# Optimization experiments

Measured on AMD Instinct MI355X. Metric: run time of the kernel, lower is better.

The kernel has to match this reference:

```python
import jax, jax.numpy as jnp
import numpy as np

B, T, D = 4, 2048, 1024
DK, DV = 1024, 1024
BETA1, BETA2 = 1.0, 1.0
EPS = 1e-12  # torch F.normalize eps


def setup_inputs() -> dict:
    key = jax.random.key(0)
    kx, kq, kk, kv, ko = jax.random.split(key, 5)
    def w(k, shape):
        return jax.random.normal(k, shape, dtype=jnp.float32) * (shape[0] ** -0.5)
    return {
        "x": jax.random.normal(kx, (B, T, D), dtype=jnp.float32),
        # Weights stored [in, out]; torch Linear is x @ W.T with W [out, in] -- equivalent math.
        "Wq": w(kq, (D, DK)),
        "Wk": w(kk, (D, DK)),
        "Wv": w(kv, (D, DV)),
        "Wo": w(ko, (DV, D)),
    }


def reference(x, Wq, Wk, Wv, Wo):
    scale = DK ** -0.5
    q = (x @ Wq) * scale                      # [B,T,DK]
    k = x @ Wk
    k = k / jnp.maximum(jnp.linalg.norm(k, axis=-1, keepdims=True), EPS)
    v = x @ Wv                                # [B,T,DV]
    # time-major for scan
    qT = jnp.swapaxes(q, 0, 1)
    kT = jnp.swapaxes(k, 0, 1)
    vT = jnp.swapaxes(v, 0, 1)
    S0 = jnp.zeros((B, DV, DK), dtype=x.dtype)

    def step(S, qkv_t):
        q_t, k_t, v_t = qkv_t                 # each [B, d]
        # S @ (I - b1 k k^T) = S - b1 (S k) k^T   (same math, rank-1 form)
        Sk = jnp.einsum('bvk,bk->bv', S, k_t)
        S = S - BETA1 * Sk[:, :, None] * k_t[:, None, :] \
              + BETA2 * v_t[:, :, None] * k_t[:, None, :]
        o_t = jnp.einsum('bvk,bk->bv', S, q_t)
        return S, o_t

    _, oT = jax.lax.scan(step, S0, (qT, kT, vT))  # oT: [T,B,DV]
    out = jnp.swapaxes(oT, 0, 1) @ Wo             # [B,T,D]
    return out
```

## Files before the change

kernel.cpp:

```cpp
#include <hip/hip_runtime.h>

typedef unsigned short u16;
typedef __attribute__((ext_vector_type(8))) short short8;
typedef __attribute__((ext_vector_type(4))) float floatx4;

#define B_ 4
#define T_ 2048
#define CH 64

__device__ __forceinline__ u16 f2bf(float f) {
  unsigned int x = __float_as_uint(f);
  return (u16)((x + 0x7FFFu + ((x >> 16) & 1u)) >> 16);
}
__device__ __forceinline__ float bf2f(u16 u) {
  union { unsigned int i; float f; } v; v.i = ((unsigned int)u) << 16; return v.f;
}

__device__ __forceinline__ void barrier_lgkm() {
  asm volatile("s_waitcnt lgkmcnt(0)\n\ts_barrier" ::: "memory");
}

#define GL(dst, addr, IMM) \
  asm volatile("global_load_dwordx4 %0, %1, off offset:" #IMM : "=v"(dst) : "v"(addr))
#define GLU(dst, addr, IMM) \
  asm volatile("global_load_ushort %0, %1, off offset:" #IMM : "=v"(dst) : "v"(addr))
#define GS(addr, val, IMM) \
  asm volatile("global_store_short %0, %1, off offset:" #IMM :: "v"(addr), "v"(val))

#define GLA(slot, base, I0, I1, I2, I3) do { \
  GL(af[slot][0], base, I0); GL(af[slot][1], base, I1); \
  GL(af[slot][2], base, I2); GL(af[slot][3], base, I3); } while (0)

#define GLKT(nt0) do { \
  const u16* kp0_ = ktb + (size_t)(nt0) * ktstep; \
  GL(ktf[nt0][0], kp0_, 0); GL(ktf[nt0][1], kp0_, 64); \
  const u16* kp1_ = ktb + (size_t)(nt0 + 1) * ktstep; \
  GL(ktf[nt0 + 1][0], kp1_, 0); GL(ktf[nt0 + 1][1], kp1_, 64); } while (0)

#define GLX4 do { \
  GL(wpf0, wrow, 0); GL(wpf1, wrow, 64); \
  GLU(vv0, vvb, 0); GLU(vv1, vvb, 2048); \
  GLU(vv2, vvb2, 0); GLU(vv3, vvb2, 2048); } while (0)

#define NOOP ((void)0)

#define AITER(K, NW, PREFETCH, XCODE) do { \
  asm volatile("s_waitcnt vmcnt(" #NW ")"); \
  __builtin_amdgcn_sched_barrier(0x387); \
  PREFETCH; \
  XCODE; \
  short8 b0_ = *reinterpret_cast<const short8*>(&Sb[l16][(K * 4 + 0) * 32 + quad * 8]); \
  short8 b1_ = *reinterpret_cast<const short8*>(&Sb[l16][(K * 4 + 1) * 32 + quad * 8]); \
  short8 b2_ = *reinterpret_cast<const short8*>(&Sb[l16][(K * 4 + 2) * 32 + quad * 8]); \
  short8 b3_ = *reinterpret_cast<const short8*>(&Sb[l16][(K * 4 + 3) * 32 + quad * 8]); \
  ac0 = __builtin_amdgcn_mfma_f32_16x16x32_bf16(af[K][0], b0_, ac0, 0, 0, 0); \
  ac1 = __builtin_amdgcn_mfma_f32_16x16x32_bf16(af[K][1], b1_, ac1, 0, 0, 0); \
  ac2 = __builtin_amdgcn_mfma_f32_16x16x32_bf16(af[K][2], b2_, ac2, 0, 0, 0); \
  ac3 = __builtin_amdgcn_mfma_f32_16x16x32_bf16(af[K][3], b3_, ac3, 0, 0, 0); \
} while (0)

__global__ __launch_bounds__(256) void xconv_kernel(const float* __restrict__ x,
                                                    u16* __restrict__ Xbf) {
  size_t idx = ((size_t)blockIdx.x * 256 + threadIdx.x) * 4;
  float4 v = *reinterpret_cast<const float4*>(&x[idx]);
  ushort4 o;
  o.x = f2bf(v.x); o.y = f2bf(v.y); o.z = f2bf(v.z); o.w = f2bf(v.w);
  *reinterpret_cast<ushort4*>(&Xbf[idx]) = o;
}

__global__ __launch_bounds__(256) void wtrans_kernel(
    const float* __restrict__ W0, const float* __restrict__ W1,
    const float* __restrict__ W2, const float* __restrict__ W3,
    u16* __restrict__ T0, u16* __restrict__ T1,
    u16* __restrict__ T2, u16* __restrict__ T3)
{
  const int z = blockIdx.z;
  const float* W = (z == 0) ? W0 : (z == 1) ? W1 : (z == 2) ? W2 : W3;
  u16* T = (z == 0) ? T0 : (z == 1) ? T1 : (z == 2) ? T2 : T3;
  const int k0 = blockIdx.x * 64, n0 = blockIdx.y * 64;
  const int tid = threadIdx.x;
  __shared__ float Tile[64][65];
#pragma unroll
  for (int i = 0; i < 4; ++i) {
    int lin = tid + i * 256;
    int r = lin >> 4, c4 = (lin & 15) * 4;
    *reinterpret_cast<float4*>(&Tile[r][c4]) =
        *reinterpret_cast<const float4*>(&W[(size_t)(k0 + r) * 1024 + n0 + c4]);
  }
  __syncthreads();
#pragma unroll
  for (int i = 0; i < 4; ++i) {
    int lin = tid + i * 256;
    int r = lin >> 4, c4 = (lin & 15) * 4;
    ushort4 o;
    o.x = f2bf(Tile[c4 + 0][r]); o.y = f2bf(Tile[c4 + 1][r]);
    o.z = f2bf(Tile[c4 + 2][r]); o.w = f2bf(Tile[c4 + 3][r]);
    *reinterpret_cast<ushort4*>(&T[(size_t)(n0 + r) * 1024 + k0 + c4]) = o;
  }
}

__global__ __launch_bounds__(256) void mgemm_qkv(
    const u16* __restrict__ Xbf,
    const u16* __restrict__ WqT, const u16* __restrict__ WkT, const u16* __restrict__ WvT,
    u16* __restrict__ Qbf, u16* __restrict__ Kbf, u16* __restrict__ Vbf,
    int tg, int lsh)
{
  const int z = blockIdx.z;
  const u16* BT = (z == 0) ? WqT : ((z == 1) ? WkT : WvT);
  u16* O = (z == 0) ? Qbf : ((z == 1) ? Kbf : Vbf);
  const float scale = (z == 0) ? 0.03125f : 1.0f;
  const int r0 = blockIdx.x * 128, c0 = blockIdx.y * 128;
// ... 100 lines not shown
        int col = c0 + wc + ni * 16 + l16;
        out[(size_t)grow * 1024 + col] = acc[mi][ni][reg];
      }
    }
}

__global__ __launch_bounds__(256) void knorm_kernel(u16* __restrict__ Kbf) {
  const int row = blockIdx.x;
  const int tid = threadIdx.x;
  ushort4 v4 = *reinterpret_cast<const ushort4*>(&Kbf[(size_t)row * 1024 + tid * 4]);
  float a = bf2f(v4.x), b = bf2f(v4.y), c = bf2f(v4.z), d = bf2f(v4.w);
  float ss = a * a + b * b + c * c + d * d;
#pragma unroll
  for (int off = 32; off > 0; off >>= 1) ss += __shfl_down(ss, off);
  __shared__ float wsum[4];
  if ((tid & 63) == 0) wsum[tid >> 6] = ss;
  __syncthreads();
  float tot = wsum[0] + wsum[1] + wsum[2] + wsum[3];
  float inv = 1.0f / fmaxf(sqrtf(tot), 1e-12f);
  ushort4 o;
  o.x = f2bf(a * inv); o.y = f2bf(b * inv); o.z = f2bf(c * inv); o.w = f2bf(d * inv);
  *reinterpret_cast<ushort4*>(&Kbf[(size_t)row * 1024 + tid * 4]) = o;
}

__global__ __launch_bounds__(256) void ktrans_kernel(const u16* __restrict__ Kbf,
                                                     u16* __restrict__ KT,
                                                     int tgs) {
  const int t0 = blockIdx.x * 64;
  const int d0 = blockIdx.y * 64;
  const int b = blockIdx.z;
  const int tid = threadIdx.x;
  __shared__ u16 Tile[64][68];
#pragma unroll
  for (int i = 0; i < 4; ++i) {
    int lin = tid + i * 256;
    int r = lin >> 4, c4 = (lin & 15) * 4;
    *reinterpret_cast<ushort4*>(&Tile[r][c4]) =
        *reinterpret_cast<const ushort4*>(&Kbf[(size_t)(b * tgs + t0 + r) * 1024 + d0 + c4]);
  }
  __syncthreads();
#pragma unroll
  for (int i = 0; i < 4; ++i) {
    int lin = tid + i * 256;
    int r = lin >> 4, c4 = (lin & 15) * 4;
    ushort4 o;
    o.x = Tile[c4 + 0][r]; o.y = Tile[c4 + 1][r];
    o.z = Tile[c4 + 2][r]; o.w = Tile[c4 + 3][r];
    *reinterpret_cast<ushort4*>(&KT[((size_t)b * 1024 + d0 + r) * tgs + t0 + c4]) = o;
  }
}

__global__ __launch_bounds__(256) void attn_winv_kernel(
    const u16* __restrict__ Qbf, const u16* __restrict__ Kbf,
    u16* __restrict__ Pb, u16* __restrict__ Wb, int tgs)
{
  const int cc = blockIdx.x;
  const int b = blockIdx.y;
  const int base = b * tgs + cc * CH;
  const int tid = threadIdx.x;
  const int lane = tid & 63;
  const int wave = tid >> 6;
  const int quad = lane >> 4, l16 = lane & 15;
  const int m0 = wave * 16;

  __shared__ float Asm[64][64];
  __shared__ float Wsm[64][65];

  floatx4 accA[4] = {};
  floatx4 accP[4] = {};
  const u16* arowK = &Kbf[(size_t)(base + m0 + l16) * 1024];
  const u16* arowQ = &Qbf[(size_t)(base + m0 + l16) * 1024];
#pragma unroll 4
  for (int kk = 0; kk < 32; ++kk) {
    short8 aK = *reinterpret_cast<const short8*>(&arowK[kk * 32 + quad * 8]);
    short8 aQ = *reinterpret_cast<const short8*>(&arowQ[kk * 32 + quad * 8]);
#pragma unroll
    for (int nt = 0; nt < 4; ++nt) {
      short8 bK = *reinterpret_cast<const short8*>(
          &Kbf[(size_t)(base + nt * 16 + l16) * 1024 + kk * 32 + quad * 8]);
      accA[nt] = __builtin_amdgcn_mfma_f32_16x16x32_bf16(aK, bK, accA[nt], 0, 0, 0);
      accP[nt] = __builtin_amdgcn_mfma_f32_16x16x32_bf16(aQ, bK, accP[nt], 0, 0, 0);
    }
  }
  const size_t pw0 = ((size_t)(cc * B_ + b) * CH) * 64;
#pragma unroll
  for (int nt = 0; nt < 4; ++nt) {
#pragma unroll
    for (int reg = 0; reg < 4; ++reg) {
      int t = m0 + quad * 4 + reg;
      int i = nt * 16 + l16;
      Asm[t][i] = (i < t) ? accA[nt][reg] : 0.0f;
      Pb[pw0 + (size_t)t * 64 + i] = f2bf((i <= t) ? accP[nt][reg] : 0.0f);
    }
  }
  __syncthreads();

  if (tid < 64) {
    const int j = tid;
    for (int t = 0; t < 64; ++t) {
      float s = (t == j) ? 1.0f : 0.0f;
      for (int i = 0; i < t; ++i) s -= Asm[t][i] * Wsm[i][j];
      Wsm[t][j] = s;
    }
    for (int t = 0; t < 64; ++t)
      Wb[pw0 + (size_t)t * 64 + j] = f2bf(Wsm[t][j]);
  }
}

__global__ __launch_bounds__(512, 2) void chain_kernel(
    const u16* __restrict__ Qbf, const u16* __restrict__ Kbf,
    const u16* __restrict__ KT, const u16* __restrict__ Vbf,
    u16* __restrict__ Obf, const u16* __restrict__ Wb, const u16* __restrict__ Pb,
    float* __restrict__ Sglob, int lsh, int cpg, int g, int ngrp)
{
  const int wg = blockIdx.x;
  const int t8 = wg & 7;
  const int b = t8 >> 1;
  const int sl = ((wg >> 3) << 1) | (t8 & 1);
  const int c0 = sl * 16;
  const int tgs = 1 << lsh;
  const int tid = threadIdx.x;
  const int lane = tid & 63;
  const int wave = tid >> 6;
  const int quad = lane >> 4, l16 = lane & 15;
  const int d0w = wave * 128;
  const bool isK = (wave < 4);
  const int m0 = (isK ? wave : (wave - 4)) * 16;
  const size_t ktstep = (size_t)16 * tgs;

  __shared__ u16 Sb[16][1048];
  __shared__ u16 rhsT[16][88];
  __shared__ u16 uT[16][88];

  floatx4 Sreg[8];
  if (g == 0) {
#pragma unroll
    for (int nt = 0; nt < 8; ++nt) Sreg[nt] = (floatx4){0.f, 0.f, 0.f, 0.f};
    for (int idx = tid; idx < 16 * 256; idx += 512) {
      int r = idx >> 8, d4 = (idx & 255) * 4;
      ushort4 z4 = {0, 0, 0, 0};
      *reinterpret_cast<ushort4*>(&Sb[r][d4]) = z4;
    }
  } else {
#pragma unroll
    for (int nt = 0; nt < 8; ++nt)
#pragma unroll
      for (int reg = 0; reg < 4; ++reg)
        Sreg[nt][reg] = Sglob[((size_t)b * 1024 + c0 + quad * 4 + reg) * 1024 +
                              d0w + nt * 16 + l16];
    for (int idx = tid; idx < 16 * 1024; idx += 512) {
      int r = idx >> 10, d = idx & 1023;
      Sb[r][d] = f2bf(Sglob[((size_t)b * 1024 + c0 + r) * 1024 + d]);
    }
  }
  __syncthreads();

  const u16* const Abase = isK ? Kbf : Qbf;
  const u16* arow = Abase + (size_t)(b * tgs + m0 + l16) * 1024;

  short8 af[8][4];
  short8 ktf[8][2];
  short8 wpf0, wpf1;
  unsigned int vv0, vv1, vv2, vv3;

  {
    const u16* aq0 = arow + quad * 8;
    GLA(0, aq0, 0, 64, 128, 192);
    GLA(1, aq0, 256, 320, 384, 448);
  }

  for (int cc = 0; cc < cpg; ++cc) {
    const int base = b * tgs + cc * CH;
    const size_t pw0 = ((size_t)(cc * B_ + b) * CH) * 64;

    const u16* aq   = arow + quad * 8;
    const u16* aqn  = arow + (size_t)(cc + 1 < cpg ? CH * 1024 : 0) + quad * 8;
    const u16* ktb  = KT + ((size_t)b * 1024 + d0w + l16) * tgs + (size_t)cc * CH + quad * 8;
    const u16* wrow = (isK ? Wb : Pb) + pw0 + (size_t)(m0 + l16) * 64 + quad * 8;
    const u16* vvb  = Vbf + (size_t)(base + m0 + quad * 4) * 1024 + c0 + l16;
    const u16* vvb2 = vvb + 2048;

    floatx4 ac0 = {}, ac1 = {}, ac2 = {}, ac3 = {};

    AITER(0, 4,  GLA(2, aq, 512, 576, 640, 704),     GLKT(0));
    AITER(1, 8,  GLA(3, aq, 768, 832, 896, 960),     GLKT(2));
    AITER(2, 12, GLA(4, aq, 1024, 1088, 1152, 1216), GLKT(4));
    AITER(3, 12, GLA(5, aq, 1280, 1344, 1408, 1472), GLKT(6));
    AITER(4, 12, GLA(6, aq, 1536, 1600, 1664, 1728), GLX4);
    AITER(5, 14, GLA(7, aq, 1792, 1856, 1920, 1984), NOOP);
    AITER(6, 10, GLA(0, aqn, 0, 64, 128, 192),       NOOP);
    AITER(7, 4,  GLA(1, aqn, 256, 320, 384, 448),    NOOP);

    asm volatile("s_waitcnt vmcnt(12)");
    __builtin_amdgcn_sched_barrier(0);

    floatx4 accS = (ac0 + ac1) + (ac2 + ac3);

    if (isK) {
      rhsT[l16][m0 + quad * 4 + 0] = f2bf(bf2f((u16)vv0) - accS[0]);
      rhsT[l16][m0 + quad * 4 + 1] = f2bf(bf2f((u16)vv1) - accS[1]);
      rhsT[l16][m0 + quad * 4 + 2] = f2bf(bf2f((u16)vv2) - accS[2]);
      rhsT[l16][m0 + quad * 4 + 3] = f2bf(bf2f((u16)vv3) - accS[3]);
    }
    barrier_lgkm();

    if (isK) {
      floatx4 uacc = {};
      short8 br0 = *reinterpret_cast<const short8*>(&rhsT[l16][quad * 8]);
      short8 br1 = *reinterpret_cast<const short8*>(&rhsT[l16][32 + quad * 8]);
      uacc = __builtin_amdgcn_mfma_f32_16x16x32_bf16(wpf0, br0, uacc, 0, 0, 0);
      uacc = __builtin_amdgcn_mfma_f32_16x16x32_bf16(wpf1, br1, uacc, 0, 0, 0);
#pragma unroll
      for (int reg = 0; reg < 4; ++reg)
        uT[l16][m0 + quad * 4 + reg] = f2bf(uacc[reg]);
    }
    barrier_lgkm();

    if (!isK) {
      floatx4 oacc = accS;
      short8 bu0 = *reinterpret_cast<const short8*>(&uT[l16][quad * 8]);
      short8 bu1 = *reinterpret_cast<const short8*>(&uT[l16][32 + quad * 8]);
      oacc = __builtin_amdgcn_mfma_f32_16x16x32_bf16(wpf0, bu0, oacc, 0, 0, 0);
      oacc = __builtin_amdgcn_mfma_f32_16x16x32_bf16(wpf1, bu1, oacc, 0, 0, 0);
      u16* ob  = Obf + (size_t)(base + m0 + quad * 4) * 1024 + c0 + l16;
      u16* ob2 = ob + 2048;
      unsigned int s0 = f2bf(oacc[0]), s1 = f2bf(oacc[1]);
      unsigned int s2 = f2bf(oacc[2]), s3 = f2bf(oacc[3]);
      GS(ob, s0, 0);  GS(ob, s1, 2048);
      GS(ob2, s2, 0); GS(ob2, s3, 2048);
    }

    {
      short8 ua0 = *reinterpret_cast<const short8*>(&uT[l16][quad * 8]);
      short8 ua1 = *reinterpret_cast<const short8*>(&uT[l16][32 + quad * 8]);
#pragma unroll
      for (int nt = 0; nt < 8; ++nt) {
        floatx4 cf = Sreg[nt];
        cf = __builtin_amdgcn_mfma_f32_16x16x32_bf16(ua0, ktf[nt][0], cf, 0, 0, 0);
        cf = __builtin_amdgcn_mfma_f32_16x16x32_bf16(ua1, ktf[nt][1], cf, 0, 0, 0);
        Sreg[nt] = cf;
        const int dn = d0w + nt * 16;
#pragma unroll
        for (int reg = 0; reg < 4; ++reg)
          Sb[quad * 4 + reg][dn + l16] = f2bf(cf[reg]);
      }
    }
    barrier_lgkm();
    arow += CH * 1024;
  }

  if (g < ngrp - 1) {
#pragma unroll
    for (int nt = 0; nt < 8; ++nt)
#pragma unroll
      for (int reg = 0; reg < 4; ++reg)
        Sglob[((size_t)b * 1024 + c0 + quad * 4 + reg) * 1024 + d0w + nt * 16 + l16] =
            Sreg[nt][reg];
  }
}

extern "C" void kernel_launch(void* const* d_in, const int* in_sizes, int n_in,
                              void* d_out, int out_size, void* d_ws, size_t ws_size,
                              hipStream_t stream) {
  const float* x  = (const float*)d_in[0];
  const float* Wq = (const float*)d_in[1];
  const float* Wk = (const float*)d_in[2];
  const float* Wv = (const float*)d_in[3];
  const float* Wo = (const float*)d_in[4];
  float* out = (float*)d_out;

  int lsh = 8;
  {
    const int cand[4] = {11, 10, 9, 8};
    for (int i = 0; i < 4; ++i) {
      size_t tgs = (size_t)1 << cand[i];
      size_t C = (size_t)B_ * tgs * 1024;
      size_t cpg = tgs / CH;
      size_t need = (size_t)B_ * T_ * 1024 * 2
                  + 4 * ((size_t)1024 * 1024 * 2)
                  + 5 * (C * 2)
                  + 2 * (cpg * B_ * CH * 64 * 2)
                  + (size_t)B_ * 1024 * 1024 * 4
                  + 32768;
      if (need <= ws_size) { lsh = cand[i]; break; }
    }
  }
  const int tgs = 1 << lsh;
  const int cpg = tgs / CH;
  const int ngrp = T_ / tgs;
  const int rows = B_ * tgs;

  char* ws = (char*)d_ws;
  size_t off = 0;
  auto alloc = [&](size_t bytes) -> void* {
    void* p = ws + off;
    off += (bytes + 255) & ~(size_t)255;
    return p;
  };
  u16* Xbf = (u16*)alloc((size_t)B_ * T_ * 1024 * 2);
  u16* WqT = (u16*)alloc((size_t)1024 * 1024 * 2);
  u16* WkT = (u16*)alloc((size_t)1024 * 1024 * 2);
  u16* WvT = (u16*)alloc((size_t)1024 * 1024 * 2);
  u16* WoT = (u16*)alloc((size_t)1024 * 1024 * 2);
  u16* Qbf = (u16*)alloc((size_t)rows * 1024 * 2);
  u16* Kbf = (u16*)alloc((size_t)rows * 1024 * 2);
  u16* Vbf = (u16*)alloc((size_t)rows * 1024 * 2);
  u16* KT  = (u16*)alloc((size_t)rows * 1024 * 2);
  u16* Obf = (u16*)alloc((size_t)rows * 1024 * 2);
  u16* Pb  = (u16*)alloc((size_t)cpg * B_ * CH * 64 * 2);
  u16* Wb  = (u16*)alloc((size_t)cpg * B_ * CH * 64 * 2);
  float* Sglob = (float*)alloc((size_t)B_ * 1024 * 1024 * 4);

  xconv_kernel<<<B_ * T_, 256, 0, stream>>>(x, Xbf);
  wtrans_kernel<<<dim3(16, 16, 4), 256, 0, stream>>>(Wq, Wk, Wv, Wo, WqT, WkT, WvT, WoT);

  for (int g = 0; g < ngrp; ++g) {
    int tg = g * tgs;
    mgemm_qkv<<<dim3(rows / 128, 8, 3), 256, 0, stream>>>(Xbf, WqT, WkT, WvT,
                                                          Qbf, Kbf, Vbf, tg, lsh);
    knorm_kernel<<<rows, 256, 0, stream>>>(Kbf);
    ktrans_kernel<<<dim3(tgs / 64, 16, B_), 256, 0, stream>>>(Kbf, KT, tgs);
    attn_winv_kernel<<<dim3(cpg, B_), 256, 0, stream>>>(Qbf, Kbf, Pb, Wb, tgs);
    chain_kernel<<<256, 512, 0, stream>>>(Qbf, Kbf, KT, Vbf, Obf, Wb, Pb, Sglob,
                                          lsh, cpg, g, ngrp);
    mgemm_out<<<dim3(rows / 128, 8), 256, 0, stream>>>(Obf, WoT, out, tg, lsh);
  }
}
```

Before: 628.1 us.

## Pipeline chunk recurrence by computing next chunk's A@S before state update using cross-chunk correction

The chain kernel now computes the next chunk's K/Q times the current state (the old S) while the rank-update of S is still being written into a double-buffered Sb. It corrects for the missing update with precomputed cross-chunk Gram blocks M=K_next·K_prev^T and N=Q_next·K_prev^T times the previous u. The attention kernel computes these extra blocks, and the next chunk's prefetch and O stores are moved to overlap with the MFMA loop. The aim is to shorten the serial critical path between chunks. The cost is extra Gram-matrix work, doubled Sb LDS use, and more workspace.

```diff
diff --git a/kernel.cpp b/kernel.cpp
--- a/kernel.cpp
+++ b/kernel.cpp
@@ -37,26 +37,73 @@
   const u16* kp1_ = ktb + (size_t)(nt0 + 1) * ktstep; \
   GL(ktf[nt0 + 1][0], kp1_, 0); GL(ktf[nt0 + 1][1], kp1_, 64); } while (0)
 
-#define GLX4 do { \
+#define GLWM do { \
   GL(wpf0, wrow, 0); GL(wpf1, wrow, 64); \
+  GL(mnf0, mnrow, 0); GL(mnf1, mnrow, 64); } while (0)
+
+#define GLVV do { \
   GLU(vv0, vvb, 0); GLU(vv1, vvb, 2048); \
   GLU(vv2, vvb2, 0); GLU(vv3, vvb2, 2048); } while (0)
 
-#define NOOP ((void)0)
-
-#define AITER(K, NW, PREFETCH, XCODE) do { \
+#define NOOP ((void)0);
+
+#define A_IT(K, NW, EXTRA) do { \
   asm volatile("s_waitcnt vmcnt(" #NW ")"); \
   __builtin_amdgcn_sched_barrier(0x387); \
-  PREFETCH; \
-  XCODE; \
-  short8 b0_ = *reinterpret_cast<const short8*>(&Sb[l16][(K * 4 + 0) * 32 + quad * 8]); \
-  short8 b1_ = *reinterpret_cast<const short8*>(&Sb[l16][(K * 4 + 1) * 32 + quad * 8]); \
-  short8 b2_ = *reinterpret_cast<const short8*>(&Sb[l16][(K * 4 + 2) * 32 + quad * 8]); \
-  short8 b3_ = *reinterpret_cast<const short8*>(&Sb[l16][(K * 4 + 3) * 32 + quad * 8]); \
+  EXTRA \
+  short8 b0_ = *reinterpret_cast<const short8*>(sbRow + (K * 4 + 0) * 32 + quad * 8); \
+  short8 b1_ = *reinterpret_cast<const short8*>(sbRow + (K * 4 + 1) * 32 + quad * 8); \
+  short8 b2_ = *reinterpret_cast<const short8*>(sbRow + (K * 4 + 2) * 32 + quad * 8); \
+  short8 b3_ = *reinterpret_cast<const short8*>(sbRow + (K * 4 + 3) * 32 + quad * 8); \
   ac0 = __builtin_amdgcn_mfma_f32_16x16x32_bf16(af[K][0], b0_, ac0, 0, 0, 0); \
   ac1 = __builtin_amdgcn_mfma_f32_16x16x32_bf16(af[K][1], b1_, ac1, 0, 0, 0); \
   ac2 = __builtin_amdgcn_mfma_f32_16x16x32_bf16(af[K][2], b2_, ac2, 0, 0, 0); \
   ac3 = __builtin_amdgcn_mfma_f32_16x16x32_bf16(af[K][3], b3_, ac3, 0, 0, 0); \
+} while (0)
+
+#define SETPTRS(N) \
+  const int nxc_ = (N); \
+  const u16* aqN = Abase + (size_t)(b * tgs + nxc_ * CH + m0 + l16) * 1024 + quad * 8; \
+  const u16* ktb = KT + ((size_t)b * 1024 + d0w + l16) * tgs + (size_t)nxc_ * CH + quad * 8; \
+  const size_t pwN = ((size_t)(nxc_ * B_ + b) * CH) * 64; \
+  const u16* wrow  = WPbase + pwN + (size_t)(m0 + l16) * 64 + quad * 8; \
+  const u16* mnrow = MNbase + pwN + (size_t)(m0 + l16) * 64 + quad * 8; \
+  const u16* vvb  = Vbf + (size_t)(b * tgs + nxc_ * CH + m0 + quad * 4) * 1024 + c0 + l16; \
+  const u16* vvb2 = vvb + 2048;
+
+#define I1I2(C) do { \
+  const int nn_ = ((C) + 1 < cpg) ? ((C) + 1) : (cpg - 1); \
+  const u16* aq2_ = Abase + (size_t)(b * tgs + nn_ * CH + m0 + l16) * 1024 + quad * 8; \
+  GLA(0, aq2_, 0, 64, 128, 192); \
+  GLA(1, aq2_, 256, 320, 384, 448); \
+  asm volatile("s_waitcnt vmcnt(8)"); \
+  __builtin_amdgcn_sched_barrier(0); \
+  accS = (ac0 + ac1) + (ac2 + ac3); \
+  { \
+    short8 cu0_ = *reinterpret_cast<const short8*>(&uT[l16][quad * 8]); \
+    short8 cu1_ = *reinterpret_cast<const short8*>(&uT[l16][32 + quad * 8]); \
+    accS = __builtin_amdgcn_mfma_f32_16x16x32_bf16(mnf0, cu0_, accS, 0, 0, 0); \
+    accS = __builtin_amdgcn_mfma_f32_16x16x32_bf16(mnf1, cu1_, accS, 0, 0, 0); \
+  } \
+  if (isK) { \
+    rhsT[l16][m0 + quad * 4 + 0] = f2bf(bf2f((u16)vv0) - accS[0]); \
+    rhsT[l16][m0 + quad * 4 + 1] = f2bf(bf2f((u16)vv1) - accS[1]); \
+    rhsT[l16][m0 + quad * 4 + 2] = f2bf(bf2f((u16)vv2) - accS[2]); \
+    rhsT[l16][m0 + quad * 4 + 3] = f2bf(bf2f((u16)vv3) - accS[3]); \
+  } \
+  barrier_lgkm(); \
+  if (isK) { \
+    floatx4 uacc = {}; \
+    short8 br0_ = *reinterpret_cast<const short8*>(&rhsT[l16][quad * 8]); \
+    short8 br1_ = *reinterpret_cast<const short8*>(&rhsT[l16][32 + quad * 8]); \
+    uacc = __builtin_amdgcn_mfma_f32_16x16x32_bf16(wpf0, br0_, uacc, 0, 0, 0); \
+    uacc = __builtin_amdgcn_mfma_f32_16x16x32_bf16(wpf1, br1_, uacc, 0, 0, 0); \
+    uT[l16][m0 + quad * 4 + 0] = f2bf(uacc[0]); \
+    uT[l16][m0 + quad * 4 + 1] = f2bf(uacc[1]); \
+    uT[l16][m0 + quad * 4 + 2] = f2bf(uacc[2]); \
+    uT[l16][m0 + quad * 4 + 3] = f2bf(uacc[3]); \
+  } \
+  barrier_lgkm(); \
 } while (0)
 
 __global__ __launch_bounds__(256) void xconv_kernel(const float* __restrict__ x,
@@ -263,11 +310,13 @@
 
 __global__ __launch_bounds__(256) void attn_winv_kernel(
     const u16* __restrict__ Qbf, const u16* __restrict__ Kbf,
-    u16* __restrict__ Pb, u16* __restrict__ Wb, int tgs)
+    u16* __restrict__ Pb, u16* __restrict__ Wb,
+    u16* __restrict__ Mb, u16* __restrict__ Nb, int tgs)
 {
   const int cc = blockIdx.x;
   const int b = blockIdx.y;
   const int base = b * tgs + cc * CH;
+  const int basep = base - (cc > 0 ? CH : 0);
   const int tid = threadIdx.x;
   const int lane = tid & 63;
   const int wave = tid >> 6;
@@ -279,9 +328,11 @@
 
   floatx4 accA[4] = {};
   floatx4 accP[4] = {};
+  floatx4 accM[4] = {};
+  floatx4 accN[4] = {};
   const u16* arowK = &Kbf[(size_t)(base + m0 + l16) * 1024];
   const u16* arowQ = &Qbf[(size_t)(base + m0 + l16) * 1024];
-#pragma unroll 4
+#pragma unroll 2
   for (int kk = 0; kk < 32; ++kk) {
     short8 aK = *reinterpret_cast<const short8*>(&arowK[kk * 32 + quad * 8]);
     short8 aQ = *reinterpret_cast<const short8*>(&arowQ[kk * 32 + quad * 8]);
@@ -292,6 +343,15 @@
       accA[nt] = __builtin_amdgcn_mfma_f32_16x16x32_bf16(aK, bK, accA[nt], 0, 0, 0);
       accP[nt] = __builtin_amdgcn_mfma_f32_16x16x32_bf16(aQ, bK, accP[nt], 0, 0, 0);
     }
+    if (cc > 0) {
+#pragma unroll
+      for (int nt = 0; nt < 4; ++nt) {
+        short8 bKp = *reinterpret_cast<const short8*>(
+            &Kbf[(size_t)(basep + nt * 16 + l16) * 1024 + kk * 32 + quad * 8]);
+        accM[nt] = __builtin_amdgcn_mfma_f32_16x16x32_bf16(aK, bKp, accM[nt], 0, 0, 0);
+        accN[nt] = __builtin_amdgcn_mfma_f32_16x16x32_bf16(aQ, bKp, accN[nt], 0, 0, 0);
+      }
+    }
   }
   const size_t pw0 = ((size_t)(cc * B_ + b) * CH) * 64;
 #pragma unroll
@@ -302,6 +362,8 @@
       int i = nt * 16 + l16;
       Asm[t][i] = (i < t) ? accA[nt][reg] : 0.0f;
       Pb[pw0 + (size_t)t * 64 + i] = f2bf((i <= t) ? accP[nt][reg] : 0.0f);
+      Mb[pw0 + (size_t)t * 64 + i] = f2bf(accM[nt][reg]);
+      Nb[pw0 + (size_t)t * 64 + i] = f2bf(accN[nt][reg]);
     }
   }
   __syncthreads();
@@ -322,6 +384,7 @@
     const u16* __restrict__ Qbf, const u16* __restrict__ Kbf,
     const u16* __restrict__ KT, const u16* __restrict__ Vbf,
     u16* __restrict__ Obf, const u16* __restrict__ Wb, const u16* __restrict__ Pb,
+    const u16* __restrict__ Mb, const u16* __restrict__ Nb,
     float* __restrict__ Sglob, int lsh, int cpg, int g, int ngrp)
 {
   const int wg = blockIdx.x;
@@ -339,9 +402,12 @@
   const int m0 = (isK ? wave : (wave - 4)) * 16;
   const size_t ktstep = (size_t)16 * tgs;
 
-  __shared__ u16 Sb[16][1048];
+  __shared__ u16 Sb[2][16][1048];
   __shared__ u16 rhsT[16][88];
   __shared__ u16 uT[16][88];
+
+  for (int i = tid; i < 16 * 88 / 2; i += 512)
+    reinterpret_cast<unsigned int*>(&uT[0][0])[i] = 0u;
 
   floatx4 Sreg[8];
   if (g == 0) {
@@ -350,7 +416,7 @@
     for (int idx = tid; idx < 16 * 256; idx += 512) {
       int r = idx >> 8, d4 = (idx & 255) * 4;
       ushort4 z4 = {0, 0, 0, 0};
-      *reinterpret_cast<ushort4*>(&Sb[r][d4]) = z4;
+      *reinterpret_cast<ushort4*>(&Sb[0][r][d4]) = z4;
     }
   } else {
 #pragma unroll
@@ -361,89 +427,63 @@
                               d0w + nt * 16 + l16];
     for (int idx = tid; idx < 16 * 1024; idx += 512) {
       int r = idx >> 10, d = idx & 1023;
-      Sb[r][d] = f2bf(Sglob[((size_t)b * 1024 + c0 + r) * 1024 + d]);
+      Sb[0][r][d] = f2bf(Sglob[((size_t)b * 1024 + c0 + r) * 1024 + d]);
     }
   }
   __syncthreads();
 
-  const u16* const Abase = isK ? Kbf : Qbf;
-  const u16* arow = Abase + (size_t)(b * tgs + m0 + l16) * 1024;
+  const u16* const Abase  = isK ? Kbf : Qbf;
+  const u16* const WPbase = isK ? Wb : Pb;
+  const u16* const MNbase = isK ? Mb : Nb;
 
   short8 af[8][4];
   short8 ktf[8][2];
-  short8 wpf0, wpf1;
+  short8 wpf0, wpf1, mnf0, mnf1;
   unsigned int vv0, vv1, vv2, vv3;
+  floatx4 ac0, ac1, ac2, ac3, accS;
 
   {
-    const u16* aq0 = arow + quad * 8;
+    const u16* aq0 = Abase + (size_t)(b * tgs + m0 + l16) * 1024 + quad * 8;
     GLA(0, aq0, 0, 64, 128, 192);
     GLA(1, aq0, 256, 320, 384, 448);
   }
+  int cur = 0;
+  {
+    SETPTRS(0);
+    const u16* sbRow = &Sb[0][l16][0];
+    ac0 = (floatx4){}; ac1 = (floatx4){}; ac2 = (floatx4){}; ac3 = (floatx4){};
+    A_IT(0, 4, GLKT(0); GLA(2, aqN, 512, 576, 640, 704););
+    A_IT(1, 8, GLKT(2); GLA(3, aqN, 768, 832, 896, 960););
+    A_IT(2, 8, GLKT(4); GLA(4, aqN, 1024, 1088, 1152, 1216););
+    A_IT(3, 8, GLKT(6); GLA(5, aqN, 1280, 1344, 1408, 1472););
+    A_IT(4, 8, GLWM; GLA(6, aqN, 1536, 1600, 1664, 1728););
+    A_IT(5, 8, GLA(7, aqN, 1792, 1856, 1920, 1984); GLVV;);
+    A_IT(6, 8, NOOP);
+    A_IT(7, 4, NOOP);
+  }
+  I1I2(0);
 
   for (int cc = 0; cc < cpg; ++cc) {
-    const int base = b * tgs + cc * CH;
-    const size_t pw0 = ((size_t)(cc * B_ + b) * CH) * 64;
-
-    const u16* aq   = arow + quad * 8;
-    const u16* aqn  = arow + (size_t)(cc + 1 < cpg ? CH * 1024 : 0) + quad * 8;
-    const u16* ktb  = KT + ((size_t)b * 1024 + d0w + l16) * tgs + (size_t)cc * CH + quad * 8;
-    const u16* wrow = (isK ? Wb : Pb) + pw0 + (size_t)(m0 + l16) * 64 + quad * 8;
-    const u16* vvb  = Vbf + (size_t)(base + m0 + quad * 4) * 1024 + c0 + l16;
-    const u16* vvb2 = vvb + 2048;
-
-    floatx4 ac0 = {}, ac1 = {}, ac2 = {}, ac3 = {};
-
-    AITER(0, 4,  GLA(2, aq, 512, 576, 640, 704),     GLKT(0));
-    AITER(1, 8,  GLA(3, aq, 768, 832, 896, 960),     GLKT(2));
-    AITER(2, 12, GLA(4, aq, 1024, 1088, 1152, 1216), GLKT(4));
-    AITER(3, 12, GLA(5, aq, 1280, 1344, 1408, 1472), GLKT(6));
-    AITER(4, 12, GLA(6, aq, 1536, 1600, 1664, 1728), GLX4);
-    AITER(5, 14, GLA(7, aq, 1792, 1856, 1920, 1984), NOOP);
-    AITER(6, 10, GLA(0, aqn, 0, 64, 128, 192),       NOOP);
-    AITER(7, 4,  GLA(1, aqn, 256, 320, 384, 448),    NOOP);
-
-    asm volatile("s_waitcnt vmcnt(12)");
-    __builtin_amdgcn_sched_barrier(0);
-
-    floatx4 accS = (ac0 + ac1) + (ac2 + ac3);
-
-    if (isK) {
-      rhsT[l16][m0 + quad * 4 + 0] = f2bf(bf2f((u16)vv0) - accS[0]);
-      rhsT[l16][m0 + quad * 4 + 1] = f2bf(bf2f((u16)vv1) - accS[1]);
-      rhsT[l16][m0 + quad * 4 + 2] = f2bf(bf2f((u16)vv2) - accS[2]);
-      rhsT[l16][m0 + quad * 4 + 3] = f2bf(bf2f((u16)vv3) - accS[3]);
-    }
-    barrier_lgkm();
-
-    if (isK) {
-      floatx4 uacc = {};
-      short8 br0 = *reinterpret_cast<const short8*>(&rhsT[l16][quad * 8]);
-      short8 br1 = *reinterpret_cast<const short8*>(&rhsT[l16][32 + quad * 8]);
-      uacc = __builtin_amdgcn_mfma_f32_16x16x32_bf16(wpf0, br0, uacc, 0, 0, 0);
-      uacc = __builtin_amdgcn_mfma_f32_16x16x32_bf16(wpf1, br1, uacc, 0, 0, 0);
-#pragma unroll
-      for (int reg = 0; reg < 4; ++reg)
-        uT[l16][m0 + quad * 4 + reg] = f2bf(uacc[reg]);
-    }
-    barrier_lgkm();
-
+    const int nx = (cc + 1 < cpg) ? (cc + 1) : (cpg - 1);
+    SETPTRS(nx);
+    const u16* sbRow = &Sb[cur][l16][0];
+
+    short8 ua0 = *reinterpret_cast<const short8*>(&uT[l16][quad * 8]);
+    short8 ua1 = *reinterpret_cast<const short8*>(&uT[l16][32 + quad * 8]);
+
+    unsigned int s0 = 0, s1 = 0, s2 = 0, s3 = 0;
+    u16* ob = nullptr; u16* ob2 = nullptr;
     if (!isK) {
       floatx4 oacc = accS;
-      short8 bu0 = *reinterpret_cast<const short8*>(&uT[l16][quad * 8]);
-      short8 bu1 = *reinterpret_cast<const short8*>(&uT[l16][32 + quad * 8]);
-      oacc = __builtin_amdgcn_mfma_f32_16x16x32_bf16(wpf0, bu0, oacc, 0, 0, 0);
-      oacc = __builtin_amdgcn_mfma_f32_16x16x32_bf16(wpf1, bu1, oacc, 0, 0, 0);
-      u16* ob  = Obf + (size_t)(base + m0 + quad * 4) * 1024 + c0 + l16;
-      u16* ob2 = ob + 2048;
-      unsigned int s0 = f2bf(oacc[0]), s1 = f2bf(oacc[1]);
-      unsigned int s2 = f2bf(oacc[2]), s3 = f2bf(oacc[3]);
-      GS(ob, s0, 0);  GS(ob, s1, 2048);
-      GS(ob2, s2, 0); GS(ob2, s3, 2048);
+      oacc = __builtin_amdgcn_mfma_f32_16x16x32_bf16(wpf0, ua0, oacc, 0, 0, 0);
+      oacc = __builtin_amdgcn_mfma_f32_16x16x32_bf16(wpf1, ua1, oacc, 0, 0, 0);
+      ob  = Obf + (size_t)(b * tgs + cc * CH + m0 + quad * 4) * 1024 + c0 + l16;
+      ob2 = ob + 2048;
+      s0 = f2bf(oacc[0]); s1 = f2bf(oacc[1]);
+      s2 = f2bf(oacc[2]); s3 = f2bf(oacc[3]);
     }
 
     {
-      short8 ua0 = *reinterpret_cast<const short8*>(&uT[l16][quad * 8]);
-      short8 ua1 = *reinterpret_cast<const short8*>(&uT[l16][32 + quad * 8]);
 #pragma unroll
       for (int nt = 0; nt < 8; ++nt) {
         floatx4 cf = Sreg[nt];
@@ -453,12 +493,31 @@
         const int dn = d0w + nt * 16;
 #pragma unroll
         for (int reg = 0; reg < 4; ++reg)
-          Sb[quad * 4 + reg][dn + l16] = f2bf(cf[reg]);
+          Sb[cur ^ 1][quad * 4 + reg][dn + l16] = f2bf(cf[reg]);
       }
     }
+
+    ac0 = (floatx4){}; ac1 = (floatx4){}; ac2 = (floatx4){}; ac3 = (floatx4){};
+    A_IT(0, 4, GLKT(0); GLA(2, aqN, 512, 576, 640, 704););
+    A_IT(1, 8, GLKT(2); GLA(3, aqN, 768, 832, 896, 960););
+    A_IT(2, 8, GLKT(4); GLA(4, aqN, 1024, 1088, 1152, 1216););
+    A_IT(3, 8, GLKT(6); GLA(5, aqN, 1280, 1344, 1408, 1472););
+    A_IT(4, 8, GLWM; GLA(6, aqN, 1536, 1600, 1664, 1728););
+    A_IT(5, 8, GLA(7, aqN, 1792, 1856, 1920, 1984); GLVV;);
+    A_IT(6, 8, NOOP);
+    A_IT(7, 4, NOOP);
+
+    if (!isK) {
+      GS(ob, s0, 0);  GS(ob, s1, 2048);
+      GS(ob2, s2, 0); GS(ob2, s3, 2048);
+    }
     barrier_lgkm();
-    arow += CH * 1024;
-  }
+    cur ^= 1;
+
+    if (cc + 1 < cpg) I1I2(cc + 1);
+  }
+
+  asm volatile("s_waitcnt vmcnt(0)");
 
   if (g < ngrp - 1) {
 #pragma unroll
@@ -490,7 +549,7 @@
       size_t need = (size_t)B_ * T_ * 1024 * 2
                   + 4 * ((size_t)1024 * 1024 * 2)
                   + 5 * (C * 2)
-                  + 2 * (cpg * B_ * CH * 64 * 2)
+                  + 4 * (cpg * B_ * CH * 64 * 2)
                   + (size_t)B_ * 1024 * 1024 * 4
                   + 32768;
       if (need <= ws_size) { lsh = cand[i]; break; }
@@ -520,6 +579,8 @@
   u16* Obf = (u16*)alloc((size_t)rows * 1024 * 2);
   u16* Pb  = (u16*)alloc((size_t)cpg * B_ * CH * 64 * 2);
   u16* Wb  = (u16*)alloc((size_t)cpg * B_ * CH * 64 * 2);
+  u16* Mb  = (u16*)alloc((size_t)cpg * B_ * CH * 64 * 2);
+  u16* Nb  = (u16*)alloc((size_t)cpg * B_ * CH * 64 * 2);
   float* Sglob = (float*)alloc((size_t)B_ * 1024 * 1024 * 4);
 
   xconv_kernel<<<B_ * T_, 256, 0, stream>>>(x, Xbf);
@@ -531,9 +592,9 @@
                                                           Qbf, Kbf, Vbf, tg, lsh);
     knorm_kernel<<<rows, 256, 0, stream>>>(Kbf);
     ktrans_kernel<<<dim3(tgs / 64, 16, B_), 256, 0, stream>>>(Kbf, KT, tgs);
-    attn_winv_kernel<<<dim3(cpg, B_), 256, 0, stream>>>(Qbf, Kbf, Pb, Wb, tgs);
-    chain_kernel<<<256, 512, 0, stream>>>(Qbf, Kbf, KT, Vbf, Obf, Wb, Pb, Sglob,
-                                          lsh, cpg, g, ngrp);
+    attn_winv_kernel<<<dim3(cpg, B_), 256, 0, stream>>>(Qbf, Kbf, Pb, Wb, Mb, Nb, tgs);
+    chain_kernel<<<256, 512, 0, stream>>>(Qbf, Kbf, KT, Vbf, Obf, Wb, Pb, Mb, Nb,
+                                          Sglob, lsh, cpg, g, ngrp);
     mgemm_out<<<dim3(rows / 128, 8), 256, 0, stream>>>(Obf, WoT, out, tg, lsh);
   }
 }
```

Result: slower. 676.8 us (+7.8%).

## Process two state slices per chain workgroup to reuse K/Q/KT loads

Applied to the files above, without the earlier changes.

Each chain workgroup now handles two 16-row slices of the state (c0 and c0+512) instead of one, halving the grid from 256 to 128 workgroups. The A fragments (K/Q rows) and KT fragments loaded from global memory are shared across both slices, halving redundant global traffic per unit of work. In exchange, register pressure and LDS use double (two Sb buffers, two Sreg sets), and fewer workgroups means lower occupancy and parallelism across the GPU.

```diff
diff --git a/kernel.cpp b/kernel.cpp
--- a/kernel.cpp
+++ b/kernel.cpp
@@ -37,26 +37,36 @@
   const u16* kp1_ = ktb + (size_t)(nt0 + 1) * ktstep; \
   GL(ktf[nt0 + 1][0], kp1_, 0); GL(ktf[nt0 + 1][1], kp1_, 64); } while (0)
 
-#define GLX4 do { \
-  GL(wpf0, wrow, 0); GL(wpf1, wrow, 64); \
-  GLU(vv0, vvb, 0); GLU(vv1, vvb, 2048); \
-  GLU(vv2, vvb2, 0); GLU(vv3, vvb2, 2048); } while (0)
-
-#define NOOP ((void)0)
-
-#define AITER(K, NW, PREFETCH, XCODE) do { \
+#define GLW do { GL(wpf0, wrow, 0); GL(wpf1, wrow, 64); } while (0)
+#define GLVVA do { \
+  GLU(vva0, vvba, 0); GLU(vva1, vvba, 2048); \
+  GLU(vva2, vvba2, 0); GLU(vva3, vvba2, 2048); } while (0)
+#define GLVVB do { \
+  GLU(vvb0, vvbb, 0); GLU(vvb1, vvbb, 2048); \
+  GLU(vvb2_, vvbb2, 0); GLU(vvb3, vvbb2, 2048); } while (0)
+
+#define NOOP ((void)0);
+
+#define A_IT(K, NW, EXTRA) do { \
   asm volatile("s_waitcnt vmcnt(" #NW ")"); \
   __builtin_amdgcn_sched_barrier(0x387); \
-  PREFETCH; \
-  XCODE; \
-  short8 b0_ = *reinterpret_cast<const short8*>(&Sb[l16][(K * 4 + 0) * 32 + quad * 8]); \
-  short8 b1_ = *reinterpret_cast<const short8*>(&Sb[l16][(K * 4 + 1) * 32 + quad * 8]); \
-  short8 b2_ = *reinterpret_cast<const short8*>(&Sb[l16][(K * 4 + 2) * 32 + quad * 8]); \
-  short8 b3_ = *reinterpret_cast<const short8*>(&Sb[l16][(K * 4 + 3) * 32 + quad * 8]); \
-  ac0 = __builtin_amdgcn_mfma_f32_16x16x32_bf16(af[K][0], b0_, ac0, 0, 0, 0); \
-  ac1 = __builtin_amdgcn_mfma_f32_16x16x32_bf16(af[K][1], b1_, ac1, 0, 0, 0); \
-  ac2 = __builtin_amdgcn_mfma_f32_16x16x32_bf16(af[K][2], b2_, ac2, 0, 0, 0); \
-  ac3 = __builtin_amdgcn_mfma_f32_16x16x32_bf16(af[K][3], b3_, ac3, 0, 0, 0); \
+  EXTRA \
+  short8 pa0_ = *reinterpret_cast<const short8*>(&Sba[l16][(K * 4 + 0) * 32 + quad * 8]); \
+  short8 pa1_ = *reinterpret_cast<const short8*>(&Sba[l16][(K * 4 + 1) * 32 + quad * 8]); \
+  short8 pa2_ = *reinterpret_cast<const short8*>(&Sba[l16][(K * 4 + 2) * 32 + quad * 8]); \
+  short8 pa3_ = *reinterpret_cast<const short8*>(&Sba[l16][(K * 4 + 3) * 32 + quad * 8]); \
+  short8 pb0_ = *reinterpret_cast<const short8*>(&Sbb[l16][(K * 4 + 0) * 32 + quad * 8]); \
+  short8 pb1_ = *reinterpret_cast<const short8*>(&Sbb[l16][(K * 4 + 1) * 32 + quad * 8]); \
+  short8 pb2_ = *reinterpret_cast<const short8*>(&Sbb[l16][(K * 4 + 2) * 32 + quad * 8]); \
+  short8 pb3_ = *reinterpret_cast<const short8*>(&Sbb[l16][(K * 4 + 3) * 32 + quad * 8]); \
+  ac0a = __builtin_amdgcn_mfma_f32_16x16x32_bf16(af[K][0], pa0_, ac0a, 0, 0, 0); \
+  ac0b = __builtin_amdgcn_mfma_f32_16x16x32_bf16(af[K][0], pb0_, ac0b, 0, 0, 0); \
+  ac1a = __builtin_amdgcn_mfma_f32_16x16x32_bf16(af[K][1], pa1_, ac1a, 0, 0, 0); \
+  ac1b = __builtin_amdgcn_mfma_f32_16x16x32_bf16(af[K][1], pb1_, ac1b, 0, 0, 0); \
+  ac2a = __builtin_amdgcn_mfma_f32_16x16x32_bf16(af[K][2], pa2_, ac2a, 0, 0, 0); \
+  ac2b = __builtin_amdgcn_mfma_f32_16x16x32_bf16(af[K][2], pb2_, ac2b, 0, 0, 0); \
+  ac3a = __builtin_amdgcn_mfma_f32_16x16x32_bf16(af[K][3], pa3_, ac3a, 0, 0, 0); \
+  ac3b = __builtin_amdgcn_mfma_f32_16x16x32_bf16(af[K][3], pb3_, ac3b, 0, 0, 0); \
 } while (0)
 
 __global__ __launch_bounds__(256) void xconv_kernel(const float* __restrict__ x,
@@ -327,8 +337,9 @@
   const int wg = blockIdx.x;
   const int t8 = wg & 7;
   const int b = t8 >> 1;
-  const int sl = ((wg >> 3) << 1) | (t8 & 1);
-  const int c0 = sl * 16;
+  const int slp = ((wg >> 3) << 1) | (t8 & 1);
+  const int c0a = slp * 16;
+  const int c0b = c0a + 512;
   const int tgs = 1 << lsh;
   const int tid = threadIdx.x;
   const int lane = tid & 63;
@@ -339,40 +350,54 @@
   const int m0 = (isK ? wave : (wave - 4)) * 16;
   const size_t ktstep = (size_t)16 * tgs;
 
-  __shared__ u16 Sb[16][1048];
-  __shared__ u16 rhsT[16][88];
-  __shared__ u16 uT[16][88];
-
-  floatx4 Sreg[8];
+  __shared__ u16 Sba[16][1048];
+  __shared__ u16 Sbb[16][1048];
+  __shared__ u16 rhsTa[16][88];
+  __shared__ u16 rhsTb[16][88];
+  __shared__ u16 uTa[16][88];
+  __shared__ u16 uTb[16][88];
+
+  floatx4 SregA[8], SregB[8];
   if (g == 0) {
 #pragma unroll
-    for (int nt = 0; nt < 8; ++nt) Sreg[nt] = (floatx4){0.f, 0.f, 0.f, 0.f};
+    for (int nt = 0; nt < 8; ++nt) {
+      SregA[nt] = (floatx4){0.f, 0.f, 0.f, 0.f};
+      SregB[nt] = (floatx4){0.f, 0.f, 0.f, 0.f};
+    }
     for (int idx = tid; idx < 16 * 256; idx += 512) {
       int r = idx >> 8, d4 = (idx & 255) * 4;
       ushort4 z4 = {0, 0, 0, 0};
-      *reinterpret_cast<ushort4*>(&Sb[r][d4]) = z4;
+      *reinterpret_cast<ushort4*>(&Sba[r][d4]) = z4;
+      *reinterpret_cast<ushort4*>(&Sbb[r][d4]) = z4;
     }
   } else {
 #pragma unroll
     for (int nt = 0; nt < 8; ++nt)
 #pragma unroll
-      for (int reg = 0; reg < 4; ++reg)
-        Sreg[nt][reg] = Sglob[((size_t)b * 1024 + c0 + quad * 4 + reg) * 1024 +
-                              d0w + nt * 16 + l16];
+      for (int reg = 0; reg < 4; ++reg) {
+        SregA[nt][reg] = Sglob[((size_t)b * 1024 + c0a + quad * 4 + reg) * 1024 +
+                               d0w + nt * 16 + l16];
+        SregB[nt][reg] = Sglob[((size_t)b * 1024 + c0b + quad * 4 + reg) * 1024 +
+                               d0w + nt * 16 + l16];
+      }
     for (int idx = tid; idx < 16 * 1024; idx += 512) {
       int r = idx >> 10, d = idx & 1023;
-      Sb[r][d] = f2bf(Sglob[((size_t)b * 1024 + c0 + r) * 1024 + d]);
+      Sba[r][d] = f2bf(Sglob[((size_t)b * 1024 + c0a + r) * 1024 + d]);
+      Sbb[r][d] = f2bf(Sglob[((size_t)b * 1024 + c0b + r) * 1024 + d]);
     }
   }
   __syncthreads();
 
-  const u16* const Abase = isK ? Kbf : Qbf;
-  const u16* arow = Abase + (size_t)(b * tgs + m0 + l16) * 1024;
+  const u16* const Abase  = isK ? Kbf : Qbf;
+  const u16* const WPbase = isK ? Wb : Pb;
 
   short8 af[8][4];
   short8 ktf[8][2];
   short8 wpf0, wpf1;
-  unsigned int vv0, vv1, vv2, vv3;
+  unsigned int vva0, vva1, vva2, vva3;
+  unsigned int vvb0, vvb1, vvb2_, vvb3;
+
+  const u16* arow = Abase + (size_t)(b * tgs + m0 + l16) * 1024;
 
   {
     const u16* aq0 = arow + quad * 8;
@@ -387,86 +412,120 @@
     const u16* aq   = arow + quad * 8;
     const u16* aqn  = arow + (size_t)(cc + 1 < cpg ? CH * 1024 : 0) + quad * 8;
     const u16* ktb  = KT + ((size_t)b * 1024 + d0w + l16) * tgs + (size_t)cc * CH + quad * 8;
-    const u16* wrow = (isK ? Wb : Pb) + pw0 + (size_t)(m0 + l16) * 64 + quad * 8;
-    const u16* vvb  = Vbf + (size_t)(base + m0 + quad * 4) * 1024 + c0 + l16;
-    const u16* vvb2 = vvb + 2048;
-
-    floatx4 ac0 = {}, ac1 = {}, ac2 = {}, ac3 = {};
-
-    AITER(0, 4,  GLA(2, aq, 512, 576, 640, 704),     GLKT(0));
-    AITER(1, 8,  GLA(3, aq, 768, 832, 896, 960),     GLKT(2));
-    AITER(2, 12, GLA(4, aq, 1024, 1088, 1152, 1216), GLKT(4));
-    AITER(3, 12, GLA(5, aq, 1280, 1344, 1408, 1472), GLKT(6));
-    AITER(4, 12, GLA(6, aq, 1536, 1600, 1664, 1728), GLX4);
-    AITER(5, 14, GLA(7, aq, 1792, 1856, 1920, 1984), NOOP);
-    AITER(6, 10, GLA(0, aqn, 0, 64, 128, 192),       NOOP);
-    AITER(7, 4,  GLA(1, aqn, 256, 320, 384, 448),    NOOP);
-
-    asm volatile("s_waitcnt vmcnt(12)");
+    const u16* wrow = WPbase + pw0 + (size_t)(m0 + l16) * 64 + quad * 8;
+    const u16* vvba  = Vbf + (size_t)(base + m0 + quad * 4) * 1024 + c0a + l16;
+    const u16* vvba2 = vvba + 2048;
+    const u16* vvbb  = Vbf + (size_t)(base + m0 + quad * 4) * 1024 + c0b + l16;
+    const u16* vvbb2 = vvbb + 2048;
+
+    floatx4 ac0a = {}, ac1a = {}, ac2a = {}, ac3a = {};
+    floatx4 ac0b = {}, ac1b = {}, ac2b = {}, ac3b = {};
+
+    A_IT(0, 4,  GLA(2, aq, 512, 576, 640, 704);     GLKT(0););
+    A_IT(1, 8,  GLA(3, aq, 768, 832, 896, 960);     GLKT(2););
+    A_IT(2, 12, GLA(4, aq, 1024, 1088, 1152, 1216); GLKT(4););
+    A_IT(3, 12, GLA(5, aq, 1280, 1344, 1408, 1472); GLKT(6););
+    A_IT(4, 12, GLA(6, aq, 1536, 1600, 1664, 1728); GLW;);
+    A_IT(5, 10, GLA(7, aq, 1792, 1856, 1920, 1984); GLVVA; GLVVB;);
+    A_IT(6, 14, GLA(0, aqn, 0, 64, 128, 192););
+    A_IT(7, 12, GLA(1, aqn, 256, 320, 384, 448););
+
+    asm volatile("s_waitcnt vmcnt(8)");
     __builtin_amdgcn_sched_barrier(0);
 
-    floatx4 accS = (ac0 + ac1) + (ac2 + ac3);
+    floatx4 accSa = (ac0a + ac1a) + (ac2a + ac3a);
+    floatx4 accSb = (ac0b + ac1b) + (ac2b + ac3b);
 
     if (isK) {
-      rhsT[l16][m0 + quad * 4 + 0] = f2bf(bf2f((u16)vv0) - accS[0]);
-      rhsT[l16][m0 + quad * 4 + 1] = f2bf(bf2f((u16)vv1) - accS[1]);
-      rhsT[l16][m0 + quad * 4 + 2] = f2bf(bf2f((u16)vv2) - accS[2]);
-      rhsT[l16][m0 + quad * 4 + 3] = f2bf(bf2f((u16)vv3) - accS[3]);
+      rhsTa[l16][m0 + quad * 4 + 0] = f2bf(bf2f((u16)vva0) - accSa[0]);
+      rhsTa[l16][m0 + quad * 4 + 1] = f2bf(bf2f((u16)vva1) - accSa[1]);
+      rhsTa[l16][m0 + quad * 4 + 2] = f2bf(bf2f((u16)vva2) - accSa[2]);
+      rhsTa[l16][m0 + quad * 4 + 3] = f2bf(bf2f((u16)vva3) - accSa[3]);
+      rhsTb[l16][m0 + quad * 4 + 0] = f2bf(bf2f((u16)vvb0) - accSb[0]);
+      rhsTb[l16][m0 + quad * 4 + 1] = f2bf(bf2f((u16)vvb1) - accSb[1]);
+      rhsTb[l16][m0 + quad * 4 + 2] = f2bf(bf2f((u16)vvb2_) - accSb[2]);
+      rhsTb[l16][m0 + quad * 4 + 3] = f2bf(bf2f((u16)vvb3) - accSb[3]);
     }
     barrier_lgkm();
 
     if (isK) {
-      floatx4 uacc = {};
-      short8 br0 = *reinterpret_cast<const short8*>(&rhsT[l16][quad * 8]);
-      short8 br1 = *reinterpret_cast<const short8*>(&rhsT[l16][32 + quad * 8]);
-      uacc = __builtin_amdgcn_mfma_f32_16x16x32_bf16(wpf0, br0, uacc, 0, 0, 0);
-      uacc = __builtin_amdgcn_mfma_f32_16x16x32_bf16(wpf1, br1, uacc, 0, 0, 0);
-#pragma unroll
-      for (int reg = 0; reg < 4; ++reg)
-        uT[l16][m0 + quad * 4 + reg] = f2bf(uacc[reg]);
+      floatx4 uaccA = {}, uaccB = {};
+      short8 bra0 = *reinterpret_cast<const short8*>(&rhsTa[l16][quad * 8]);
+      short8 bra1 = *reinterpret_cast<const short8*>(&rhsTa[l16][32 + quad * 8]);
+      short8 brb0 = *reinterpret_cast<const short8*>(&rhsTb[l16][quad * 8]);
+      short8 brb1 = *reinterpret_cast<const short8*>(&rhsTb[l16][32 + quad * 8]);
+      uaccA = __builtin_amdgcn_mfma_f32_16x16x32_bf16(wpf0, bra0, uaccA, 0, 0, 0);
+      uaccA = __builtin_amdgcn_mfma_f32_16x16x32_bf16(wpf1, bra1, uaccA, 0, 0, 0);
+      uaccB = __builtin_amdgcn_mfma_f32_16x16x32_bf16(wpf0, brb0, uaccB, 0, 0, 0);
+      uaccB = __builtin_amdgcn_mfma_f32_16x16x32_bf16(wpf1, brb1, uaccB, 0, 0, 0);
+#pragma unroll
+      for (int reg = 0; reg < 4; ++reg) {
+        uTa[l16][m0 + quad * 4 + reg] = f2bf(uaccA[reg]);
+        uTb[l16][m0 + quad * 4 + reg] = f2bf(uaccB[reg]);
+      }
     }
     barrier_lgkm();
 
+    short8 ua0a = *reinterpret_cast<const short8*>(&uTa[l16][quad * 8]);
+    short8 ua1a = *reinterpret_cast<const short8*>(&uTa[l16][32 + quad * 8]);
+    short8 ua0b = *reinterpret_cast<const short8*>(&uTb[l16][quad * 8]);
+    short8 ua1b = *reinterpret_cast<const short8*>(&uTb[l16][32 + quad * 8]);
+
     if (!isK) {
-      floatx4 oacc = accS;
-      short8 bu0 = *reinterpret_cast<const short8*>(&uT[l16][quad * 8]);
-      short8 bu1 = *reinterpret_cast<const short8*>(&uT[l16][32 + quad * 8]);
-      oacc = __builtin_amdgcn_mfma_f32_16x16x32_bf16(wpf0, bu0, oacc, 0, 0, 0);
-      oacc = __builtin_amdgcn_mfma_f32_16x16x32_bf16(wpf1, bu1, oacc, 0, 0, 0);
-      u16* ob  = Obf + (size_t)(base + m0 + quad * 4) * 1024 + c0 + l16;
-      u16* ob2 = ob + 2048;
-      unsigned int s0 = f2bf(oacc[0]), s1 = f2bf(oacc[1]);
-      unsigned int s2 = f2bf(oacc[2]), s3 = f2bf(oacc[3]);
-      GS(ob, s0, 0);  GS(ob, s1, 2048);
-      GS(ob2, s2, 0); GS(ob2, s3, 2048);
+      floatx4 oaccA = accSa, oaccB = accSb;
+      oaccA = __builtin_amdgcn_mfma_f32_16x16x32_bf16(wpf0, ua0a, oaccA, 0, 0, 0);
+      oaccA = __builtin_amdgcn_mfma_f32_16x16x32_bf16(wpf1, ua1a, oaccA, 0, 0, 0);
+      oaccB = __builtin_amdgcn_mfma_f32_16x16x32_bf16(wpf0, ua0b, oaccB, 0, 0, 0);
+      oaccB = __builtin_amdgcn_mfma_f32_16x16x32_bf16(wpf1, ua1b, oaccB, 0, 0, 0);
+      u16* oba  = Obf + (size_t)(base + m0 + quad * 4) * 1024 + c0a + l16;
+      u16* oba2 = oba + 2048;
+      u16* obb  = Obf + (size_t)(base + m0 + quad * 4) * 1024 + c0b + l16;
+      u16* obb2 = obb + 2048;
+      unsigned int sa0 = f2bf(oaccA[0]), sa1 = f2bf(oaccA[1]);
+      unsigned int sa2 = f2bf(oaccA[2]), sa3 = f2bf(oaccA[3]);
+      unsigned int sb0 = f2bf(oaccB[0]), sb1 = f2bf(oaccB[1]);
+      unsigned int sb2 = f2bf(oaccB[2]), sb3 = f2bf(oaccB[3]);
+      GS(oba, sa0, 0);  GS(oba, sa1, 2048);
+      GS(oba2, sa2, 0); GS(oba2, sa3, 2048);
+      GS(obb, sb0, 0);  GS(obb, sb1, 2048);
+      GS(obb2, sb2, 0); GS(obb2, sb3, 2048);
     }
 
     {
-      short8 ua0 = *reinterpret_cast<const short8*>(&uT[l16][quad * 8]);
-      short8 ua1 = *reinterpret_cast<const short8*>(&uT[l16][32 + quad * 8]);
 #pragma unroll
       for (int nt = 0; nt < 8; ++nt) {
-        floatx4 cf = Sreg[nt];
-        cf = __builtin_amdgcn_mfma_f32_16x16x32_bf16(ua0, ktf[nt][0], cf, 0, 0, 0);
-        cf = __builtin_amdgcn_mfma_f32_16x16x32_bf16(ua1, ktf[nt][1], cf, 0, 0, 0);
-        Sreg[nt] = cf;
+        floatx4 ca = SregA[nt];
+        ca = __builtin_amdgcn_mfma_f32_16x16x32_bf16(ua0a, ktf[nt][0], ca, 0, 0, 0);
+        ca = __builtin_amdgcn_mfma_f32_16x16x32_bf16(ua1a, ktf[nt][1], ca, 0, 0, 0);
+        SregA[nt] = ca;
+        floatx4 cb = SregB[nt];
+        cb = __builtin_amdgcn_mfma_f32_16x16x32_bf16(ua0b, ktf[nt][0], cb, 0, 0, 0);
+        cb = __builtin_amdgcn_mfma_f32_16x16x32_bf16(ua1b, ktf[nt][1], cb, 0, 0, 0);
+        SregB[nt] = cb;
         const int dn = d0w + nt * 16;
 #pragma unroll
-        for (int reg = 0; reg < 4; ++reg)
-          Sb[quad * 4 + reg][dn + l16] = f2bf(cf[reg]);
+        for (int reg = 0; reg < 4; ++reg) {
+          Sba[quad * 4 + reg][dn + l16] = f2bf(ca[reg]);
+          Sbb[quad * 4 + reg][dn + l16] = f2bf(cb[reg]);
+        }
       }
     }
     barrier_lgkm();
     arow += CH * 1024;
   }
 
+  asm volatile("s_waitcnt vmcnt(0)");
+
   if (g < ngrp - 1) {
 #pragma unroll
     for (int nt = 0; nt < 8; ++nt)
 #pragma unroll
-      for (int reg = 0; reg < 4; ++reg)
-        Sglob[((size_t)b * 1024 + c0 + quad * 4 + reg) * 1024 + d0w + nt * 16 + l16] =
-            Sreg[nt][reg];
+      for (int reg = 0; reg < 4; ++reg) {
+        Sglob[((size_t)b * 1024 + c0a + quad * 4 + reg) * 1024 + d0w + nt * 16 + l16] =
+            SregA[nt][reg];
+        Sglob[((size_t)b * 1024 + c0b + quad * 4 + reg) * 1024 + d0w + nt * 16 + l16] =
+            SregB[nt][reg];
+      }
   }
 }
 
@@ -532,7 +591,7 @@
     knorm_kernel<<<rows, 256, 0, stream>>>(Kbf);
     ktrans_kernel<<<dim3(tgs / 64, 16, B_), 256, 0, stream>>>(Kbf, KT, tgs);
     attn_winv_kernel<<<dim3(cpg, B_), 256, 0, stream>>>(Qbf, Kbf, Pb, Wb, tgs);
-    chain_kernel<<<256, 512, 0, stream>>>(Qbf, Kbf, KT, Vbf, Obf, Wb, Pb, Sglob,
+    chain_kernel<<<128, 512, 0, stream>>>(Qbf, Kbf, KT, Vbf, Obf, Wb, Pb, Sglob,
                                           lsh, cpg, g, ngrp);
     mgemm_out<<<dim3(rows / 128, 8), 256, 0, stream>>>(Obf, WoT, out, tg, lsh);
   }
```

Result: slower. 657.0 us (+4.6%).
